# Optimization experiments

Hardware: AMD Instinct MI355X
Metric: run time of the kernel (lower is better)

## Reference

```python
import jax, jax.numpy as jnp
import numpy as np

HEADS = 8
DIM_HEAD = 64
SCALE = DIM_HEAD ** -0.5
LN_EPS = 1e-5

def setup_inputs() -> dict:
    key = jax.random.key(0)
    k0, k1, k2 = jax.random.split(key, 3)
    B, S, D = 4, 2048, 512
    inner = HEADS * DIM_HEAD
    return {
        "x": jax.random.normal(k0, (B, S, D), dtype=jnp.float32),
        "ln_gamma": jnp.ones((D,), dtype=jnp.float32),
        "ln_beta": jnp.zeros((D,), dtype=jnp.float32),
        "w_qkv": jax.random.normal(k1, (D, 3 * inner), dtype=jnp.float32) * (D ** -0.5),
        "w_out": jax.random.normal(k2, (inner, D), dtype=jnp.float32) * (inner ** -0.5),
        "b_out": jnp.zeros((D,), dtype=jnp.float32),
    }

def reference(x, ln_gamma, ln_beta, w_qkv, w_out, b_out):
    B, S, D = x.shape
    # LayerNorm
    mu = jnp.mean(x, axis=-1, keepdims=True)
    var = jnp.mean(jnp.square(x - mu), axis=-1, keepdims=True)
    xn = (x - mu) * jax.lax.rsqrt(var + LN_EPS) * ln_gamma + ln_beta
    # QKV projection (no bias)
    qkv = xn @ w_qkv  # [B, S, 3*inner]
    q, k, v = jnp.split(qkv, 3, axis=-1)
    def to_heads(t):
        return t.reshape(B, S, HEADS, DIM_HEAD).transpose(0, 2, 1, 3)  # [B,H,S,Dh]
    q, k, v = to_heads(q), to_heads(k), to_heads(v)
    # Naive attention with materialized score matrix
    dots = jnp.einsum("bhsd,bhtd->bhst", q, k) * SCALE
    attn = jax.nn.softmax(dots, axis=-1)
    out = jnp.einsum("bhst,bhtd->bhsd", attn, v)
    out = out.transpose(0, 2, 1, 3).reshape(B, S, HEADS * DIM_HEAD)
    return out @ w_out + b_out
```

## Files before the change

kernel.cpp:

```cpp
#include <hip/hip_runtime.h>
#include <hip/hip_bf16.h>
#include <stdint.h>

typedef __bf16 bf16;
typedef __bf16 bf16x8 __attribute__((ext_vector_type(8)));
typedef __bf16 bf16x4 __attribute__((ext_vector_type(4)));
typedef float  f32x4  __attribute__((ext_vector_type(4)));

#define MFMA16(A, B, C) __builtin_amdgcn_mfma_f32_16x16x32_bf16((A), (B), (C), 0, 0, 0)

static constexpr int Bsz = 4, Seq = 2048, Dm = 512, Hh = 8, Dh = 64;

__device__ __forceinline__ void g2l_16(void* lds, const void* gp) {
  __builtin_amdgcn_global_load_lds((__attribute__((address_space(1))) void*)gp,
                                   (__attribute__((address_space(3))) void*)lds, 16, 0, 0);
}

__device__ __forceinline__ float max3f(float a, float b, float c) {
  return fmaxf(fmaxf(a, b), c);
}

__global__ __launch_bounds__(256) void ln_cast_kernel(
    const float* __restrict__ x, const float* __restrict__ g,
    const float* __restrict__ be, bf16* __restrict__ xn) {
  const int row  = blockIdx.x * 4 + (threadIdx.x >> 6);
  const int lane = threadIdx.x & 63;
  const f32x4* xr = (const f32x4*)(x + (size_t)row * Dm);
  f32x4 v0 = xr[lane];
  f32x4 v1 = xr[lane + 64];
  float s = (v0.x + v0.y + v0.z + v0.w) + (v1.x + v1.y + v1.z + v1.w);
#pragma unroll
  for (int off = 32; off > 0; off >>= 1) s += __shfl_xor(s, off);
  const float mu = s * (1.0f / Dm);
  f32x4 d0 = v0 - mu, d1 = v1 - mu;
  float q = d0.x * d0.x + d0.y * d0.y + d0.z * d0.z + d0.w * d0.w
          + d1.x * d1.x + d1.y * d1.y + d1.z * d1.z + d1.w * d1.w;
#pragma unroll
  for (int off = 32; off > 0; off >>= 1) q += __shfl_xor(q, off);
  const float rs = rsqrtf(q * (1.0f / Dm) + 1e-5f);
  const f32x4* gr = (const f32x4*)g;
  const f32x4* br = (const f32x4*)be;
  f32x4 g0 = gr[lane], g1 = gr[lane + 64];
  f32x4 b0 = br[lane], b1 = br[lane + 64];
  f32x4 y0 = d0 * rs * g0 + b0;
  f32x4 y1 = d1 * rs * g1 + b1;
  bf16x4 o0 = { (bf16)y0.x, (bf16)y0.y, (bf16)y0.z, (bf16)y0.w };
  bf16x4 o1 = { (bf16)y1.x, (bf16)y1.y, (bf16)y1.z, (bf16)y1.w };
  bf16x4* orow = (bf16x4*)(xn + (size_t)row * Dm);
  orow[lane]      = o0;
  orow[lane + 64] = o1;
}

__global__ __launch_bounds__(256) void tcast_kernel(
    const float* __restrict__ src, bf16* __restrict__ dst, int R, int C,
    int qrows, float qscale) {
  __shared__ float t[32][33];
  const int c0 = blockIdx.x * 32, r0 = blockIdx.y * 32;
  const int tx = threadIdx.x & 31, ty = threadIdx.x >> 5;
#pragma unroll
  for (int i = 0; i < 32; i += 8)
    t[ty + i][tx] = src[(size_t)(r0 + ty + i) * C + c0 + tx];
  __syncthreads();
#pragma unroll
  for (int i = 0; i < 32; i += 8) {
    const int rr = c0 + ty + i;
    const float sc = rr < qrows ? qscale : 1.0f;
    dst[(size_t)rr * R + r0 + tx] = (bf16)(t[tx][ty + i] * sc);
  }
}

__global__ __launch_bounds__(256) void gemm_qkv_kernel(
    const bf16* __restrict__ A,
    const bf16* __restrict__ Bt,
    bf16* __restrict__ Qb, bf16* __restrict__ Kb, bf16* __restrict__ VT) {
  constexpr int K = 512;
  __shared__ __align__(16) bf16 As[128 * 32];
  __shared__ __align__(16) bf16 Bs[128 * 32];
  const int m0 = blockIdx.x * 128, n0 = blockIdx.y * 128;
  const int tid = threadIdx.x, lane = tid & 63, wave = tid >> 6;
  const int lr = lane & 15, lg = lane >> 4;
  const int wm = (wave >> 1) * 64, wn = (wave & 1) * 64;
  const int srow = wave * 16 + (lane >> 2);
  const int scol = (lane & 3) * 8;
  const bf16* ga = A  + (size_t)(m0 + srow) * K + scol;
  const bf16* gb = Bt + (size_t)(n0 + srow) * K + scol;
  bf16* lA = As + wave * 512;
  bf16* lB = Bs + wave * 512;
  f32x4 acc[4][4] = {};
  for (int k0 = 0; k0 < K; k0 += 32) {
    g2l_16(lA,        ga + k0);
    g2l_16(lA + 2048, ga + (size_t)64 * K + k0);
    g2l_16(lB,        gb + k0);
    g2l_16(lB + 2048, gb + (size_t)64 * K + k0);
    asm volatile("s_waitcnt vmcnt(0)" ::: "memory");
    __syncthreads();
    bf16x8 af[4], bfr[4];
#pragma unroll
    for (int i = 0; i < 4; ++i)
      af[i] = *(const bf16x8*)&As[(wm + i * 16 + lr) * 32 + lg * 8];
#pragma unroll
    for (int j = 0; j < 4; ++j)
      bfr[j] = *(const bf16x8*)&Bs[(wn + j * 16 + lr) * 32 + lg * 8];
#pragma unroll
    for (int i = 0; i < 4; ++i)
#pragma unroll
      for (int j = 0; j < 4; ++j)
        acc[i][j] = MFMA16(af[i], bfr[j], acc[i][j]);
    __syncthreads();
  }
#pragma unroll
  for (int j = 0; j < 4; ++j) {
    const int n = n0 + wn + j * 16 + lr;
    const int which = n >> 9, h = (n >> 6) & 7, dh = n & 63;
    if (which < 2) {
      bf16* dst = which == 0 ? Qb : Kb;
#pragma unroll
      for (int i = 0; i < 4; ++i)
#pragma unroll
        for (int r = 0; r < 4; ++r) {
          const int m = m0 + wm + i * 16 + lg * 4 + r;
          const int b = m >> 11, s2 = m & 2047;
          dst[((size_t)((b * Hh + h) * Seq + s2) << 6) | dh] = (bf16)acc[i][j][r];
        }
    } else {
#pragma unroll
      for (int i = 0; i < 4; ++i)
#pragma unroll
        for (int r = 0; r < 4; ++r) {
          const int m = m0 + wm + i * 16 + lg * 4 + r;
          const int b = m >> 11, s2 = m & 2047;
          VT[((size_t)((b * Hh + h) * Dh + dh)) * Seq + s2] = (bf16)acc[i][j][r];
        }
    }
  }
}

__global__ __launch_bounds__(256) void gemm_out_kernel(
    const bf16* __restrict__ A,
    const bf16* __restrict__ Bt,
    const float* __restrict__ bias, float* __restrict__ out) {
  constexpr int K = 512;
  __shared__ __align__(16) bf16 As[128 * 32];
  __shared__ __align__(16) bf16 Bs[128 * 32];
  const int m0 = blockIdx.x * 128, n0 = blockIdx.y * 128;
  const int tid = threadIdx.x, lane = tid & 63, wave = tid >> 6;
  const int lr = lane & 15, lg = lane >> 4;
  const int wm = (wave >> 1) * 64, wn = (wave & 1) * 64;
  const int srow = wave * 16 + (lane >> 2);
  const int scol = (lane & 3) * 8;
  const bf16* ga = A  + (size_t)(m0 + srow) * K + scol;
  const bf16* gb = Bt + (size_t)(n0 + srow) * K + scol;
  bf16* lA = As + wave * 512;
  bf16* lB = Bs + wave * 512;
  f32x4 acc[4][4] = {};
  for (int k0 = 0; k0 < K; k0 += 32) {
    g2l_16(lA,        ga + k0);
    g2l_16(lA + 2048, ga + (size_t)64 * K + k0);
    g2l_16(lB,        gb + k0);
    g2l_16(lB + 2048, gb + (size_t)64 * K + k0);
    asm volatile("s_waitcnt vmcnt(0)" ::: "memory");
    __syncthreads();
    bf16x8 af[4], bfr[4];
#pragma unroll
    for (int i = 0; i < 4; ++i)
      af[i] = *(const bf16x8*)&As[(wm + i * 16 + lr) * 32 + lg * 8];
#pragma unroll
    for (int j = 0; j < 4; ++j)
      bfr[j] = *(const bf16x8*)&Bs[(wn + j * 16 + lr) * 32 + lg * 8];
#pragma unroll
    for (int i = 0; i < 4; ++i)
#pragma unroll
      for (int j = 0; j < 4; ++j)
        acc[i][j] = MFMA16(af[i], bfr[j], acc[i][j]);
    __syncthreads();
  }
#pragma unroll
  for (int j = 0; j < 4; ++j) {
    const int n = n0 + wn + j * 16 + lr;
    const float bv = bias[n];
#pragma unroll
    for (int i = 0; i < 4; ++i)
#pragma unroll
      for (int r = 0; r < 4; ++r) {
        const int m = m0 + wm + i * 16 + lg * 4 + r;
        out[(size_t)m * 512 + n] = acc[i][j][r] + bv;
      }
  }
}

__global__ __launch_bounds__(512) void attn5_kernel(
    const bf16* __restrict__ Qb, const bf16* __restrict__ Kb,
    const bf16* __restrict__ VT, bf16* __restrict__ A2) {
  const int o   = blockIdx.x + gridDim.x * blockIdx.y;
  const int nid = ((o & 7) << 6) + (o >> 3);
  const int qc = nid & 15, bh = nid >> 4;
  const int b = bh >> 3, h = bh & 7;
  const int tid = threadIdx.x, lane = tid & 63, wave = tid >> 6;
  const int lr = lane & 15, lg = lane >> 4;
  const int q0 = qc * 128 + wave * 16;
  const bf16* Qh = Qb + (size_t)bh * Seq * Dh;
  const bf16* Kh = Kb + (size_t)bh * Seq * Dh;
  const bf16* Vh = VT + (size_t)bh * Dh * Seq;

  __shared__ __align__(16) bf16 KV[2][8192];
  __shared__ __align__(16) bf16 Pl[8][16][72];

  const int xs   = lr & 7;
  const int col0 = (lg ^ xs) * 8;
  const bf16* kv  = &KV[0][0];
  const int kb0 = lr * 64 + col0;
  const int kb1 = lr * 64 + (col0 ^ 32);
  bf16* pw = &Pl[wave][lr][lg * 4];
  const bf16* pr = &Pl[wave][lr][lg * 8];

  const int krow = tid >> 3;
  const int kc   = (((tid & 7) ^ (krow & 7)) * 8);
  const bf16* gK = Kh + (size_t)krow * 64 + kc;
  const bf16* gV = Vh + (size_t)krow * Seq + kc;
  bf16* ldsD = &KV[0][0] + tid * 8;

  bf16x8 qf0 = *(const bf16x8*)&Qh[(size_t)(q0 + lr) * 64 + lg * 8];
  bf16x8 qf1 = *(const bf16x8*)&Qh[(size_t)(q0 + lr) * 64 + 32 + lg * 8];

  f32x4 oa[4] = {};
  f32x4 ol = {};
  float m = -1e30f;
  bf16x8 ones;
#pragma unroll
  for (int i = 0; i < 8; ++i) ones[i] = (bf16)1.0f;

  auto TILE = [&](int buf) {
    const int kB = buf * 8192;
    f32x4 st[4] = {};
#pragma unroll
    for (int c = 0; c < 4; ++c) {
      bf16x8 kf0 = *(const bf16x8*)&kv[kb0 + kB + c * 1024];
      bf16x8 kf1 = *(const bf16x8*)&kv[kb1 + kB + c * 1024];
      st[c] = MFMA16(kf0, qf0, st[c]);
      st[c] = MFMA16(kf1, qf1, st[c]);
    }
    float m0 = max3f(st[0][0], st[0][1], st[0][2]);
    float m1 = max3f(st[0][3], st[1][0], st[1][1]);
    float m2 = max3f(st[1][2], st[1][3], st[2][0]);
    float m3 = max3f(st[2][1], st[2][2], st[2][3]);
    float m4 = max3f(st[3][0], st[3][1], st[3][2]);
    float mx = max3f(max3f(m0, m1, m2), m3, fmaxf(m4, st[3][3]));
    mx = fmaxf(mx, __shfl_xor(mx, 16));
    mx = fmaxf(mx, __shfl_xor(mx, 32));
    if (__any(mx > m + 3.0f)) {
      const float mn = fmaxf(m, mx);
      const float al = exp2f(m - mn);
      m = mn;
#pragma unroll
      for (int j = 0; j < 4; ++j) {
        const float aj = __shfl(al, lg * 4 + j);
        ol[j] *= aj;
#pragma unroll
        for (int n = 0; n < 4; ++n) oa[n][j] *= aj;
      }
    }
#pragma unroll
    for (int c = 0; c < 4; ++c) {
      bf16x4 pk;
#pragma unroll
      for (int j = 0; j < 4; ++j) pk[j] = (bf16)exp2f(st[c][j] - m);
      *(bf16x4*)&pw[c * 16] = pk;
    }
    bf16x8 pf0 = *(const bf16x8*)&pr[0];
    bf16x8 pf1 = *(const bf16x8*)&pr[32];
    ol = MFMA16(pf0, ones, ol);
    ol = MFMA16(pf1, ones, ol);
#pragma unroll
    for (int n = 0; n < 4; ++n) {
      bf16x8 vf0 = *(const bf16x8*)&kv[kb0 + kB + 4096 + n * 1024];
      bf16x8 vf1 = *(const bf16x8*)&kv[kb1 + kB + 4096 + n * 1024];
      oa[n] = MFMA16(pf0, vf0, oa[n]);
      oa[n] = MFMA16(pf1, vf1, oa[n]);
    }
  };

  g2l_16(ldsD,        gK);
  g2l_16(ldsD + 4096, gV);
  gK += 4096; gV += 64;
  asm volatile("s_waitcnt vmcnt(0)" ::: "memory");
  __syncthreads();

  for (int it = 0; it < 16; ++it) {
    g2l_16(ldsD + 8192,        gK);
    g2l_16(ldsD + 8192 + 4096, gV);
    gK += 4096; gV += 64;
    TILE(0);
    asm volatile("s_waitcnt vmcnt(0)" ::: "memory");
    __syncthreads();
    if (it < 15) {
      g2l_16(ldsD,        gK);
      g2l_16(ldsD + 4096, gV);
      gK += 4096; gV += 64;
    }
    TILE(1);
    asm volatile("s_waitcnt vmcnt(0)" ::: "memory");
    __syncthreads();
  }

#pragma unroll
  for (int j = 0; j < 4; ++j) {
    const float lj = 1.0f / ol[j];
    const int s2 = q0 + lg * 4 + j;
#pragma unroll
    for (int n = 0; n < 4; ++n)
      A2[(size_t)(b * Seq + s2) * 512 + h * 64 + n * 16 + lr] = (bf16)(oa[n][j] * lj);
  }
}

extern "C" void kernel_launch(void* const* d_in, const int* in_sizes, int n_in,
                              void* d_out, int out_size, void* d_ws, size_t ws_size,
                              hipStream_t stream) {
  const float* x    = (const float*)d_in[0];
  const float* gam  = (const float*)d_in[1];
  const float* bet  = (const float*)d_in[2];
  const float* wqkv = (const float*)d_in[3];
  const float* wout = (const float*)d_in[4];
  const float* bout = (const float*)d_in[5];
  float* out = (float*)d_out;

  bf16* xn    = (bf16*)d_ws;
  bf16* wqkvT = xn    + (size_t)8192 * 512;
  bf16* woutT = wqkvT + (size_t)1536 * 512;
  bf16* Qb    = woutT + (size_t)512 * 512;
  bf16* Kb    = Qb    + (size_t)4 * 8 * 2048 * 64;
  bf16* VT    = Kb    + (size_t)4 * 8 * 2048 * 64;
  bf16* A2    = xn;

  const float K1 = 0.18033688011112042f;

  ln_cast_kernel<<<2048, 256, 0, stream>>>(x, gam, bet, xn);
  tcast_kernel<<<dim3(48, 16), 256, 0, stream>>>(wqkv, wqkvT, 512, 1536, 512, K1);
  tcast_kernel<<<dim3(16, 16), 256, 0, stream>>>(wout, woutT, 512, 512, 0, 1.0f);
  gemm_qkv_kernel<<<dim3(64, 12), 256, 0, stream>>>(xn, wqkvT, Qb, Kb, VT);
  attn5_kernel<<<dim3(16, 32), 512, 0, stream>>>(Qb, Kb, VT, A2);
  gemm_out_kernel<<<dim3(64, 4), 256, 0, stream>>>(A2, woutT, bout, out);
}
```

Before: 109.2 us.

## Process two query blocks per wave in attention, halving block threads

The attention kernel now runs 4 waves of 256 threads per block instead of 8, and each wave handles 32 query rows split into two 16-row sub-blocks. Each K/V fragment read from LDS now feeds twice as many MFMAs, which cuts LDS read traffic per unit of compute. Tile staging becomes four 16-byte loads per thread, and s_setprio brackets the MFMA sections. The cost is more registers per wave (doubled accumulators and scores) and fewer waves available to hide latency.

Result: slower. 117.3 us (+7.4%).

```diff
diff --git a/kernel.cpp b/kernel.cpp
--- a/kernel.cpp
+++ b/kernel.cpp
@@ -188,7 +188,7 @@
   }
 }
 
-__global__ __launch_bounds__(512) void attn5_kernel(
+__global__ __launch_bounds__(256) void attn6_kernel(
     const bf16* __restrict__ Qb, const bf16* __restrict__ Kb,
     const bf16* __restrict__ VT, bf16* __restrict__ A2) {
   const int o   = blockIdx.x + gridDim.x * blockIdx.y;
@@ -197,21 +197,23 @@
   const int b = bh >> 3, h = bh & 7;
   const int tid = threadIdx.x, lane = tid & 63, wave = tid >> 6;
   const int lr = lane & 15, lg = lane >> 4;
-  const int q0 = qc * 128 + wave * 16;
+  const int q0 = qc * 128 + wave * 32;
   const bf16* Qh = Qb + (size_t)bh * Seq * Dh;
   const bf16* Kh = Kb + (size_t)bh * Seq * Dh;
   const bf16* Vh = VT + (size_t)bh * Dh * Seq;
 
   __shared__ __align__(16) bf16 KV[2][8192];
-  __shared__ __align__(16) bf16 Pl[8][16][72];
+  __shared__ __align__(16) bf16 Pl[4][2][16][72];
 
   const int xs   = lr & 7;
   const int col0 = (lg ^ xs) * 8;
-  const bf16* kv  = &KV[0][0];
+  const bf16* kv = &KV[0][0];
   const int kb0 = lr * 64 + col0;
   const int kb1 = lr * 64 + (col0 ^ 32);
-  bf16* pw = &Pl[wave][lr][lg * 4];
-  const bf16* pr = &Pl[wave][lr][lg * 8];
+  bf16* pw0 = &Pl[wave][0][lr][lg * 4];
+  bf16* pw1 = &Pl[wave][1][lr][lg * 4];
+  const bf16* pr0 = &Pl[wave][0][lr][lg * 8];
+  const bf16* pr1 = &Pl[wave][1][lr][lg * 8];
 
   const int krow = tid >> 3;
   const int kc   = (((tid & 7) ^ (krow & 7)) * 8);
@@ -219,96 +221,120 @@
   const bf16* gV = Vh + (size_t)krow * Seq + kc;
   bf16* ldsD = &KV[0][0] + tid * 8;
 
-  bf16x8 qf0 = *(const bf16x8*)&Qh[(size_t)(q0 + lr) * 64 + lg * 8];
-  bf16x8 qf1 = *(const bf16x8*)&Qh[(size_t)(q0 + lr) * 64 + 32 + lg * 8];
-
-  f32x4 oa[4] = {};
-  f32x4 ol = {};
-  float m = -1e30f;
+  bf16x8 qf[2][2];
+#pragma unroll
+  for (int qb = 0; qb < 2; ++qb) {
+    qf[qb][0] = *(const bf16x8*)&Qh[(size_t)(q0 + qb * 16 + lr) * 64 + lg * 8];
+    qf[qb][1] = *(const bf16x8*)&Qh[(size_t)(q0 + qb * 16 + lr) * 64 + 32 + lg * 8];
+  }
+
+  f32x4 oa[2][4] = {};
+  f32x4 ol[2] = {};
+  float m[2] = { -1e30f, -1e30f };
   bf16x8 ones;
 #pragma unroll
   for (int i = 0; i < 8; ++i) ones[i] = (bf16)1.0f;
+
+  auto STAGE = [&](int dstOff, int t0) {
+    g2l_16(ldsD + dstOff,        gK + (size_t)t0 * 64);
+    g2l_16(ldsD + dstOff + 2048, gK + (size_t)t0 * 64 + 2048);
+    g2l_16(ldsD + dstOff + 4096, gV + t0);
+    g2l_16(ldsD + dstOff + 6144, gV + (size_t)32 * Seq + t0);
+  };
 
   auto TILE = [&](int buf) {
     const int kB = buf * 8192;
-    f32x4 st[4] = {};
+    f32x4 st[2][4] = {};
+    __builtin_amdgcn_s_setprio(1);
 #pragma unroll
     for (int c = 0; c < 4; ++c) {
       bf16x8 kf0 = *(const bf16x8*)&kv[kb0 + kB + c * 1024];
       bf16x8 kf1 = *(const bf16x8*)&kv[kb1 + kB + c * 1024];
-      st[c] = MFMA16(kf0, qf0, st[c]);
-      st[c] = MFMA16(kf1, qf1, st[c]);
-    }
-    float m0 = max3f(st[0][0], st[0][1], st[0][2]);
-    float m1 = max3f(st[0][3], st[1][0], st[1][1]);
-    float m2 = max3f(st[1][2], st[1][3], st[2][0]);
-    float m3 = max3f(st[2][1], st[2][2], st[2][3]);
-    float m4 = max3f(st[3][0], st[3][1], st[3][2]);
-    float mx = max3f(max3f(m0, m1, m2), m3, fmaxf(m4, st[3][3]));
-    mx = fmaxf(mx, __shfl_xor(mx, 16));
-    mx = fmaxf(mx, __shfl_xor(mx, 32));
-    if (__any(mx > m + 3.0f)) {
-      const float mn = fmaxf(m, mx);
-      const float al = exp2f(m - mn);
-      m = mn;
-#pragma unroll
-      for (int j = 0; j < 4; ++j) {
-        const float aj = __shfl(al, lg * 4 + j);
-        ol[j] *= aj;
-#pragma unroll
-        for (int n = 0; n < 4; ++n) oa[n][j] *= aj;
+      st[0][c] = MFMA16(kf0, qf[0][0], st[0][c]);
+      st[0][c] = MFMA16(kf1, qf[0][1], st[0][c]);
+      st[1][c] = MFMA16(kf0, qf[1][0], st[1][c]);
+      st[1][c] = MFMA16(kf1, qf[1][1], st[1][c]);
+    }
+    __builtin_amdgcn_s_setprio(0);
+#pragma unroll
+    for (int qb = 0; qb < 2; ++qb) {
+      float m0 = max3f(st[qb][0][0], st[qb][0][1], st[qb][0][2]);
+      float m1 = max3f(st[qb][0][3], st[qb][1][0], st[qb][1][1]);
+      float m2 = max3f(st[qb][1][2], st[qb][1][3], st[qb][2][0]);
+      float m3 = max3f(st[qb][2][1], st[qb][2][2], st[qb][2][3]);
+      float m4 = max3f(st[qb][3][0], st[qb][3][1], st[qb][3][2]);
+      float mx = max3f(max3f(m0, m1, m2), m3, fmaxf(m4, st[qb][3][3]));
+      mx = fmaxf(mx, __shfl_xor(mx, 16));
+      mx = fmaxf(mx, __shfl_xor(mx, 32));
+      if (__any(mx > m[qb] + 3.0f)) {
+        const float mn = fmaxf(m[qb], mx);
+        const float al = exp2f(m[qb] - mn);
+        m[qb] = mn;
+#pragma unroll
+        for (int j = 0; j < 4; ++j) {
+          const float aj = __shfl(al, lg * 4 + j);
+          ol[qb][j] *= aj;
+#pragma unroll
+          for (int n = 0; n < 4; ++n) oa[qb][n][j] *= aj;
+        }
       }
-    }
-#pragma unroll
-    for (int c = 0; c < 4; ++c) {
-      bf16x4 pk;
-#pragma unroll
-      for (int j = 0; j < 4; ++j) pk[j] = (bf16)exp2f(st[c][j] - m);
-      *(bf16x4*)&pw[c * 16] = pk;
-    }
-    bf16x8 pf0 = *(const bf16x8*)&pr[0];
-    bf16x8 pf1 = *(const bf16x8*)&pr[32];
-    ol = MFMA16(pf0, ones, ol);
-    ol = MFMA16(pf1, ones, ol);
+      bf16* pw = qb ? pw1 : pw0;
+#pragma unroll
+      for (int c = 0; c < 4; ++c) {
+        bf16x4 pk;
+#pragma unroll
+        for (int j = 0; j < 4; ++j) pk[j] = (bf16)exp2f(st[qb][c][j] - m[qb]);
+        *(bf16x4*)&pw[c * 16] = pk;
+      }
+    }
+    bf16x8 pf[2][2];
+    pf[0][0] = *(const bf16x8*)&pr0[0];
+    pf[0][1] = *(const bf16x8*)&pr0[32];
+    pf[1][0] = *(const bf16x8*)&pr1[0];
+    pf[1][1] = *(const bf16x8*)&pr1[32];
+    __builtin_amdgcn_s_setprio(1);
+    ol[0] = MFMA16(pf[0][0], ones, ol[0]);
+    ol[0] = MFMA16(pf[0][1], ones, ol[0]);
+    ol[1] = MFMA16(pf[1][0], ones, ol[1]);
+    ol[1] = MFMA16(pf[1][1], ones, ol[1]);
 #pragma unroll
     for (int n = 0; n < 4; ++n) {
       bf16x8 vf0 = *(const bf16x8*)&kv[kb0 + kB + 4096 + n * 1024];
       bf16x8 vf1 = *(const bf16x8*)&kv[kb1 + kB + 4096 + n * 1024];
-      oa[n] = MFMA16(pf0, vf0, oa[n]);
-      oa[n] = MFMA16(pf1, vf1, oa[n]);
-    }
+      oa[0][n] = MFMA16(pf[0][0], vf0, oa[0][n]);
+      oa[0][n] = MFMA16(pf[0][1], vf1, oa[0][n]);
+      oa[1][n] = MFMA16(pf[1][0], vf0, oa[1][n]);
+      oa[1][n] = MFMA16(pf[1][1], vf1, oa[1][n]);
+    }
+    __builtin_amdgcn_s_setprio(0);
   };
 
-  g2l_16(ldsD,        gK);
-  g2l_16(ldsD + 4096, gV);
-  gK += 4096; gV += 64;
+  STAGE(0, 0);
   asm volatile("s_waitcnt vmcnt(0)" ::: "memory");
   __syncthreads();
 
   for (int it = 0; it < 16; ++it) {
-    g2l_16(ldsD + 8192,        gK);
-    g2l_16(ldsD + 8192 + 4096, gV);
-    gK += 4096; gV += 64;
+    const int t0 = it * 128;
+    STAGE(8192, t0 + 64);
     TILE(0);
     asm volatile("s_waitcnt vmcnt(0)" ::: "memory");
     __syncthreads();
-    if (it < 15) {
-      g2l_16(ldsD,        gK);
-      g2l_16(ldsD + 4096, gV);
-      gK += 4096; gV += 64;
-    }
+    if (it < 15) STAGE(0, t0 + 128);
     TILE(1);
     asm volatile("s_waitcnt vmcnt(0)" ::: "memory");
     __syncthreads();
   }
 
 #pragma unroll
-  for (int j = 0; j < 4; ++j) {
-    const float lj = 1.0f / ol[j];
-    const int s2 = q0 + lg * 4 + j;
-#pragma unroll
-    for (int n = 0; n < 4; ++n)
-      A2[(size_t)(b * Seq + s2) * 512 + h * 64 + n * 16 + lr] = (bf16)(oa[n][j] * lj);
+  for (int qb = 0; qb < 2; ++qb) {
+#pragma unroll
+    for (int j = 0; j < 4; ++j) {
+      const float lj = 1.0f / ol[qb][j];
+      const int s2 = q0 + qb * 16 + lg * 4 + j;
+#pragma unroll
+      for (int n = 0; n < 4; ++n)
+        A2[(size_t)(b * Seq + s2) * 512 + h * 64 + n * 16 + lr] = (bf16)(oa[qb][n][j] * lj);
+    }
   }
 }
 
@@ -337,6 +363,6 @@
   tcast_kernel<<<dim3(48, 16), 256, 0, stream>>>(wqkv, wqkvT, 512, 1536, 512, K1);
   tcast_kernel<<<dim3(16, 16), 256, 0, stream>>>(wout, woutT, 512, 512, 0, 1.0f);
   gemm_qkv_kernel<<<dim3(64, 12), 256, 0, stream>>>(xn, wqkvT, Qb, Kb, VT);
-  attn5_kernel<<<dim3(16, 32), 512, 0, stream>>>(Qb, Kb, VT, A2);
+  attn6_kernel<<<dim3(16, 32), 256, 0, stream>>>(Qb, Kb, VT, A2);
   gemm_out_kernel<<<dim3(64, 4), 256, 0, stream>>>(A2, woutT, bout, out);
 }
```

## Split attention KV range across two blocks with 1024-thread CTAs and combine kernel

Applied to the files above, without the earlier changes.

The attention kernel now uses 1024-thread blocks covering 256 queries each, and every block handles only half the key/value sequence (split-K), so the grid stays at 512 blocks. Each block writes a normalized partial output plus its running max and sum, and a new combine kernel merges the two halves with log-sum-exp rescaling into the head-interleaved A2 layout. This halves per-block K/V streaming and shares each staged K/V tile across twice as many waves. In exchange it adds partial-output traffic to global memory and an extra kernel launch.

New measurement: 142.6 us. +30.5%, slower.

```diff
diff --git a/kernel.cpp b/kernel.cpp
--- a/kernel.cpp
+++ b/kernel.cpp
@@ -188,36 +188,43 @@
   }
 }
 
-__global__ __launch_bounds__(512) void attn5_kernel(
+__global__ __launch_bounds__(1024, 8) void attn8_kernel(
     const bf16* __restrict__ Qb, const bf16* __restrict__ Kb,
-    const bf16* __restrict__ VT, bf16* __restrict__ A2) {
+    const bf16* __restrict__ VT, bf16* __restrict__ OPn, float2* __restrict__ ML) {
   const int o   = blockIdx.x + gridDim.x * blockIdx.y;
   const int nid = ((o & 7) << 6) + (o >> 3);
-  const int qc = nid & 15, bh = nid >> 4;
-  const int b = bh >> 3, h = bh & 7;
+  const int qs = nid & 15, bh = nid >> 4;
+  const int qc = qs >> 1, sp = qs & 1;
   const int tid = threadIdx.x, lane = tid & 63, wave = tid >> 6;
   const int lr = lane & 15, lg = lane >> 4;
-  const int q0 = qc * 128 + wave * 16;
+  const int q0 = qc * 256 + wave * 16;
   const bf16* Qh = Qb + (size_t)bh * Seq * Dh;
   const bf16* Kh = Kb + (size_t)bh * Seq * Dh;
   const bf16* Vh = VT + (size_t)bh * Dh * Seq;
 
   __shared__ __align__(16) bf16 KV[2][8192];
-  __shared__ __align__(16) bf16 Pl[8][16][72];
+  __shared__ __align__(16) bf16 Pl[16][16][72];
 
   const int xs   = lr & 7;
   const int col0 = (lg ^ xs) * 8;
-  const bf16* kv  = &KV[0][0];
+  const bf16* kv = &KV[0][0];
   const int kb0 = lr * 64 + col0;
   const int kb1 = lr * 64 + (col0 ^ 32);
   bf16* pw = &Pl[wave][lr][lg * 4];
   const bf16* pr = &Pl[wave][lr][lg * 8];
 
-  const int krow = tid >> 3;
-  const int kc   = (((tid & 7) ^ (krow & 7)) * 8);
-  const bf16* gK = Kh + (size_t)krow * 64 + kc;
-  const bf16* gV = Vh + (size_t)krow * Seq + kc;
+  const int t8   = tid & 511;
+  const int krow = t8 >> 3;
+  const int kc   = (((t8 & 7) ^ (krow & 7)) * 8);
+  const bf16* gsrc = (tid < 512)
+      ? (Kh + (size_t)(sp * 1024 + krow) * 64 + kc)
+      : (Vh + (size_t)krow * Seq + sp * 1024 + kc);
+  const int gstep = (tid < 512) ? 4096 : 64;
   bf16* ldsD = &KV[0][0] + tid * 8;
+
+  auto STAGE = [&](int dstOff, int tIdx) {
+    g2l_16(ldsD + dstOff, gsrc + (size_t)tIdx * gstep);
+  };
 
   bf16x8 qf0 = *(const bf16x8*)&Qh[(size_t)(q0 + lr) * 64 + lg * 8];
   bf16x8 qf1 = *(const bf16x8*)&Qh[(size_t)(q0 + lr) * 64 + 32 + lg * 8];
@@ -279,24 +286,16 @@
     }
   };
 
-  g2l_16(ldsD,        gK);
-  g2l_16(ldsD + 4096, gV);
-  gK += 4096; gV += 64;
+  STAGE(0, 0);
   asm volatile("s_waitcnt vmcnt(0)" ::: "memory");
   __syncthreads();
 
-  for (int it = 0; it < 16; ++it) {
-    g2l_16(ldsD + 8192,        gK);
-    g2l_16(ldsD + 8192 + 4096, gV);
-    gK += 4096; gV += 64;
+  for (int it = 0; it < 8; ++it) {
+    STAGE(8192, 2 * it + 1);
     TILE(0);
     asm volatile("s_waitcnt vmcnt(0)" ::: "memory");
     __syncthreads();
-    if (it < 15) {
-      g2l_16(ldsD,        gK);
-      g2l_16(ldsD + 4096, gV);
-      gK += 4096; gV += 64;
-    }
+    if (it < 7) STAGE(0, 2 * it + 2);
     TILE(1);
     asm volatile("s_waitcnt vmcnt(0)" ::: "memory");
     __syncthreads();
@@ -304,12 +303,33 @@
 
 #pragma unroll
   for (int j = 0; j < 4; ++j) {
+    const float mj = __shfl(m, lg * 4 + j);
     const float lj = 1.0f / ol[j];
     const int s2 = q0 + lg * 4 + j;
+    const size_t row = (size_t)bh * Seq + s2;
 #pragma unroll
     for (int n = 0; n < 4; ++n)
-      A2[(size_t)(b * Seq + s2) * 512 + h * 64 + n * 16 + lr] = (bf16)(oa[n][j] * lj);
-  }
+      OPn[((size_t)sp << 22) + row * 64 + n * 16 + lr] = (bf16)(oa[n][j] * lj);
+    if (lr == 0) ML[(sp << 16) + row] = make_float2(mj, ol[j]);
+  }
+}
+
+__global__ __launch_bounds__(256) void attn_combine_kernel(
+    const bf16* __restrict__ OPn, const float2* __restrict__ ML,
+    bf16* __restrict__ A2) {
+  const int r = blockIdx.x * 4 + (threadIdx.x >> 6);
+  const int d = threadIdx.x & 63;
+  const float2 ml0 = ML[r];
+  const float2 ml1 = ML[65536 + r];
+  const float M  = fmaxf(ml0.x, ml1.x);
+  const float a0 = exp2f(ml0.x - M) * ml0.y;
+  const float a1 = exp2f(ml1.x - M) * ml1.y;
+  const float inv = 1.0f / (a0 + a1);
+  const float v0 = (float)OPn[(size_t)r * 64 + d];
+  const float v1 = (float)OPn[(size_t)(1 << 22) + (size_t)r * 64 + d];
+  const int bh = r >> 11, s = r & 2047;
+  const int b = bh >> 3, h = bh & 7;
+  A2[(size_t)(b * Seq + s) * 512 + h * 64 + d] = (bf16)((a0 * v0 + a1 * v1) * inv);
 }
 
 extern "C" void kernel_launch(void* const* d_in, const int* in_sizes, int n_in,
@@ -329,6 +349,8 @@
   bf16* Qb    = woutT + (size_t)512 * 512;
   bf16* Kb    = Qb    + (size_t)4 * 8 * 2048 * 64;
   bf16* VT    = Kb    + (size_t)4 * 8 * 2048 * 64;
+  bf16* OPn   = VT    + (size_t)4 * 8 * 2048 * 64;
+  float2* ML  = (float2*)(OPn + ((size_t)2 << 22));
   bf16* A2    = xn;
 
   const float K1 = 0.18033688011112042f;
@@ -337,6 +359,7 @@
   tcast_kernel<<<dim3(48, 16), 256, 0, stream>>>(wqkv, wqkvT, 512, 1536, 512, K1);
   tcast_kernel<<<dim3(16, 16), 256, 0, stream>>>(wout, woutT, 512, 512, 0, 1.0f);
   gemm_qkv_kernel<<<dim3(64, 12), 256, 0, stream>>>(xn, wqkvT, Qb, Kb, VT);
-  attn5_kernel<<<dim3(16, 32), 512, 0, stream>>>(Qb, Kb, VT, A2);
+  attn8_kernel<<<dim3(16, 32), 1024, 0, stream>>>(Qb, Kb, VT, OPn, ML);
+  attn_combine_kernel<<<16384, 256, 0, stream>>>(OPn, ML, A2);
   gemm_out_kernel<<<dim3(64, 4), 256, 0, stream>>>(A2, woutT, bout, out);
 }
```

## Triple-buffer K/V tiles in attention with partial vmcnt waits

Applied to the files above, without the earlier changes.

The attention kernel moves from a double-buffered to a triple-buffered LDS K/V pipeline. Loads are issued two tiles ahead, and each step waits with vmcnt(2) instead of vmcnt(0), so one tile's global-to-LDS copy stays in flight while the current tile is computed. A raw s_barrier after an lgkmcnt wait guards the write-after-read hazard on the reused buffer. This raises LDS use per block, which could limit occupancy.

Measured after the change: 110.2 us. About the same (+0.9%).

```diff
diff --git a/kernel.cpp b/kernel.cpp
--- a/kernel.cpp
+++ b/kernel.cpp
@@ -188,7 +188,7 @@
   }
 }
 
-__global__ __launch_bounds__(512) void attn5_kernel(
+__global__ __launch_bounds__(512) void attn13_kernel(
     const bf16* __restrict__ Qb, const bf16* __restrict__ Kb,
     const bf16* __restrict__ VT, bf16* __restrict__ A2) {
   const int o   = blockIdx.x + gridDim.x * blockIdx.y;
@@ -202,12 +202,12 @@
   const bf16* Kh = Kb + (size_t)bh * Seq * Dh;
   const bf16* Vh = VT + (size_t)bh * Dh * Seq;
 
-  __shared__ __align__(16) bf16 KV[2][8192];
+  __shared__ __align__(16) bf16 KV[3][8192];
   __shared__ __align__(16) bf16 Pl[8][16][72];
 
   const int xs   = lr & 7;
   const int col0 = (lg ^ xs) * 8;
-  const bf16* kv  = &KV[0][0];
+  const bf16* kv = &KV[0][0];
   const int kb0 = lr * 64 + col0;
   const int kb1 = lr * 64 + (col0 ^ 32);
   bf16* pw = &Pl[wave][lr][lg * 4];
@@ -218,6 +218,21 @@
   const bf16* gK = Kh + (size_t)krow * 64 + kc;
   const bf16* gV = Vh + (size_t)krow * Seq + kc;
   bf16* ldsD = &KV[0][0] + tid * 8;
+
+  auto STAGE = [&](int dstOff, int t) {
+    g2l_16(ldsD + dstOff,        gK + (size_t)t * 4096);
+    g2l_16(ldsD + dstOff + 4096, gV + t * 64);
+  };
+  auto FENCE_V2 = [&]() {
+    asm volatile("s_waitcnt vmcnt(2)" ::: "memory");
+    __builtin_amdgcn_s_barrier();
+    __builtin_amdgcn_sched_barrier(0);
+  };
+  auto FENCE_WAR = [&]() {
+    asm volatile("s_waitcnt lgkmcnt(0)" ::: "memory");
+    __builtin_amdgcn_s_barrier();
+    __builtin_amdgcn_sched_barrier(0);
+  };
 
   bf16x8 qf0 = *(const bf16x8*)&Qh[(size_t)(q0 + lr) * 64 + lg * 8];
   bf16x8 qf1 = *(const bf16x8*)&Qh[(size_t)(q0 + lr) * 64 + 32 + lg * 8];
@@ -279,28 +294,30 @@
     }
   };
 
-  g2l_16(ldsD,        gK);
-  g2l_16(ldsD + 4096, gV);
-  gK += 4096; gV += 64;
+  STAGE(0, 0);
+  STAGE(8192, 1);
+
+  for (int k = 0; k < 10; ++k) {
+    const int t = k * 3;
+    STAGE(16384, t + 2);
+    FENCE_V2();
+    TILE(0);
+    FENCE_WAR();
+    STAGE(0, t + 3);
+    FENCE_V2();
+    TILE(1);
+    FENCE_WAR();
+    STAGE(8192, t + 4);
+    FENCE_V2();
+    TILE(2);
+    FENCE_WAR();
+  }
   asm volatile("s_waitcnt vmcnt(0)" ::: "memory");
-  __syncthreads();
-
-  for (int it = 0; it < 16; ++it) {
-    g2l_16(ldsD + 8192,        gK);
-    g2l_16(ldsD + 8192 + 4096, gV);
-    gK += 4096; gV += 64;
-    TILE(0);
-    asm volatile("s_waitcnt vmcnt(0)" ::: "memory");
-    __syncthreads();
-    if (it < 15) {
-      g2l_16(ldsD,        gK);
-      g2l_16(ldsD + 4096, gV);
-      gK += 4096; gV += 64;
-    }
-    TILE(1);
-    asm volatile("s_waitcnt vmcnt(0)" ::: "memory");
-    __syncthreads();
-  }
+  __builtin_amdgcn_s_barrier();
+  __builtin_amdgcn_sched_barrier(0);
+  TILE(0);
+  FENCE_WAR();
+  TILE(1);
 
 #pragma unroll
   for (int j = 0; j < 4; ++j) {
@@ -337,6 +354,6 @@
   tcast_kernel<<<dim3(48, 16), 256, 0, stream>>>(wqkv, wqkvT, 512, 1536, 512, K1);
   tcast_kernel<<<dim3(16, 16), 256, 0, stream>>>(wout, woutT, 512, 512, 0, 1.0f);
   gemm_qkv_kernel<<<dim3(64, 12), 256, 0, stream>>>(xn, wqkvT, Qb, Kb, VT);
-  attn5_kernel<<<dim3(16, 32), 512, 0, stream>>>(Qb, Kb, VT, A2);
+  attn13_kernel<<<dim3(16, 32), 512, 0, stream>>>(Qb, Kb, VT, A2);
   gemm_out_kernel<<<dim3(64, 4), 256, 0, stream>>>(A2, woutT, bout, out);
 }
```
